# Optimization experiments

Hardware: AMD Instinct MI355X
Metric: run time of the kernel (lower is better)

## Reference

```python
import jax, jax.numpy as jnp
import numpy as np

N = 50000
E = 800000
IN_DIM = 128
HID_DIM = 128
OUT_DIM = 128
EPS = 1e-5


def setup_inputs() -> dict:
    key = jax.random.key(0)
    ks = jax.random.split(key, 6)
    x = jax.random.normal(ks[0], (N, IN_DIM), dtype=jnp.float32)
    src = jax.random.randint(ks[1], (E,), 0, N, dtype=jnp.int32)
    dst = jax.random.randint(ks[2], (E,), 0, N, dtype=jnp.int32)
    W1 = jax.random.normal(ks[3], (IN_DIM, HID_DIM), dtype=jnp.float32) / np.sqrt(IN_DIM)
    W2 = jax.random.normal(ks[4], (HID_DIM, OUT_DIM), dtype=jnp.float32) / np.sqrt(HID_DIM)
    return {
        "x": x, "src": src, "dst": dst,
        "W1": W1, "b1": jnp.zeros((HID_DIM,), jnp.float32),
        "gamma1": jnp.ones((HID_DIM,), jnp.float32), "beta1": jnp.zeros((HID_DIM,), jnp.float32),
        "W2": W2, "b2": jnp.zeros((OUT_DIM,), jnp.float32),
        "gamma2": jnp.ones((OUT_DIM,), jnp.float32), "beta2": jnp.zeros((OUT_DIM,), jnp.float32),
    }


def _degrees(src, dst, n):
    ones = jnp.ones(src.shape[0], jnp.float32)
    out_deg = jax.ops.segment_sum(ones, src, num_segments=n)
    in_deg = jax.ops.segment_sum(ones, dst, num_segments=n)
    # DGL norm='both' clamps degree to min 1 before pow(-0.5)
    return jnp.clip(out_deg, 1.0) ** -0.5, jnp.clip(in_deg, 1.0) ** -0.5


def _gconv(h, src, dst, d_out, d_in, W, b):
    h = h * d_out[:, None]                                   # [N, d] src-side norm
    m = jax.ops.segment_sum(h[src], dst, num_segments=h.shape[0])  # SpMM aggregate
    m = m * d_in[:, None]                                    # dst-side norm
    return m @ W + b


def _bn(h, gamma, beta):
    mu = jnp.mean(h, axis=0)
    var = jnp.var(h, axis=0)  # biased, matches torch BN training forward
    return gamma * (h - mu) * jax.lax.rsqrt(var + EPS) + beta


def reference(x, src, dst, W1, b1, gamma1, beta1, W2, b2, gamma2, beta2):
    d_out, d_in = _degrees(src, dst, x.shape[0])
    h1 = jax.nn.relu(_bn(_gconv(x, src, dst, d_out, d_in, W1, b1), gamma1, beta1))
    # dropout is identity in eval mode
    h2 = _bn(_gconv(h1, src, dst, d_out, d_in, W2, b2), gamma2, beta2)
    return jax.nn.relu(h2 + h1)
```

## Files before the change

### kernel.cpp

```cpp
#include <hip/hip_runtime.h>
#include <hip/hip_fp16.h>

#define NODES 50000
#define EDGES 800000
#define DIM 128
#define EPS_BN 1e-5f
#define SCAN_B 1024
#define SCAN_NB ((NODES + SCAN_B - 1) / SCAN_B)
#define GEMM_NB ((NODES + 63) / 64)
#define NCH 64
#define CHE (EDGES / NCH)
#define NR 4
#define RNG (NODES / NR)

typedef _Float16 half8 __attribute__((ext_vector_type(8)));
typedef float floatx4 __attribute__((ext_vector_type(4)));

__global__ __launch_bounds__(256) void hist_part_kernel(const int* __restrict__ src,
                                                        const int* __restrict__ dst,
                                                        unsigned short* __restrict__ Psrc,
                                                        unsigned short* __restrict__ Pdst) {
    __shared__ int h[RNG];
    int chunk = blockIdx.x & (NCH - 1);
    int range = blockIdx.x >> 6;
    const int* arr = blockIdx.y ? dst : src;
    unsigned short* P = blockIdx.y ? Pdst : Psrc;
    int base = range * RNG;
    for (int i = threadIdx.x; i < RNG; i += 256) h[i] = 0;
    __syncthreads();
    int e0 = chunk * CHE;
    for (int e = e0 + threadIdx.x; e < e0 + CHE; e += 256) {
        unsigned r = (unsigned)(arr[e] - base);
        if (r < (unsigned)RNG) atomicAdd(&h[r], 1);
    }
    __syncthreads();
    for (int i = threadIdx.x; i < RNG; i += 256)
        P[(size_t)chunk * NODES + base + i] = (unsigned short)h[i];
}

__global__ __launch_bounds__(256) void combine_kernel(const unsigned short* __restrict__ Psrc,
                                                      unsigned short* __restrict__ Pdst,
                                                      int* __restrict__ cnt_in,
                                                      float* __restrict__ dn_out,
                                                      float* __restrict__ dn_in) {
    int v = blockIdx.x * 256 + threadIdx.x;
    if (v >= NODES) return;
    int s = 0;
    #pragma unroll 8
    for (int j = 0; j < NCH; ++j) s += Psrc[(size_t)j * NODES + v];
    dn_out[v] = rsqrtf((float)max(s, 1));
    int run = 0;
    for (int j = 0; j < NCH; ++j) {
        int t = Pdst[(size_t)j * NODES + v];
        Pdst[(size_t)j * NODES + v] = (unsigned short)run;
        run += t;
    }
    cnt_in[v] = run;
    dn_in[v] = rsqrtf((float)max(run, 1));
}

__global__ __launch_bounds__(SCAN_B) void scan_p1_kernel(const int* __restrict__ cnt,
                                                         int* __restrict__ row_ptr,
                                                         int* __restrict__ blk_sums) {
    __shared__ int sm[SCAN_B];
    int t = threadIdx.x;
    int idx = blockIdx.x * SCAN_B + t;
    int v = (idx < NODES) ? cnt[idx] : 0;
    sm[t] = v;
    __syncthreads();
    #pragma unroll
    for (int off = 1; off < SCAN_B; off <<= 1) {
        int u = (t >= off) ? sm[t - off] : 0;
        __syncthreads();
        sm[t] += u;
        __syncthreads();
    }
    if (idx < NODES) row_ptr[idx] = sm[t] - v;
    if (t == SCAN_B - 1) blk_sums[blockIdx.x] = sm[t];
}

__global__ __launch_bounds__(64) void scan_p2_kernel(const int* __restrict__ blk_sums,
                                                     int* __restrict__ blk_off) {
    int t = threadIdx.x;
    int orig = (t < SCAN_NB) ? blk_sums[t] : 0;
    int v = orig;
    #pragma unroll
    for (int off = 1; off < 64; off <<= 1) {
        int u = __shfl_up(v, off);
        if (t >= off) v += u;
    }
    if (t < SCAN_NB) blk_off[t] = v - orig;
}

__global__ __launch_bounds__(SCAN_B) void scan_p3_kernel(int* __restrict__ row_ptr,
                                                         const int* __restrict__ blk_off) {
    int t = threadIdx.x;
    int idx = blockIdx.x * SCAN_B + t;
    if (idx < NODES) row_ptr[idx] += blk_off[blockIdx.x];
    if (idx == 0) row_ptr[NODES] = EDGES;
}

__global__ __launch_bounds__(256) void fill_kernel(const int* __restrict__ src,
                                                   const int* __restrict__ dst,
                                                   const int* __restrict__ row_ptr,
                                                   const unsigned short* __restrict__ Pdst,
                                                   int* __restrict__ csr_src) {
    __shared__ int h[RNG];
    int chunk = blockIdx.x & (NCH - 1);
    int range = blockIdx.x >> 6;
    int base = range * RNG;
    for (int i = threadIdx.x; i < RNG; i += 256) h[i] = 0;
    __syncthreads();
    int e0 = chunk * CHE;
    const unsigned short* Pj = Pdst + (size_t)chunk * NODES;
    for (int e = e0 + threadIdx.x; e < e0 + CHE; e += 256) {
        int d = dst[e];
        unsigned r = (unsigned)(d - base);
        if (r < (unsigned)RNG) {
            int local = atomicAdd(&h[r], 1);
            csr_src[row_ptr[d] + (int)Pj[d] + local] = src[e];
        }
    }
}

__global__ __launch_bounds__(256) void w2h_kernel(const float* __restrict__ W,
                                                  __half* __restrict__ WhT) {
    int idx = blockIdx.x * 256 + threadIdx.x;
    int n = idx >> 7;
    int k = idx & 127;
    WhT[idx] = __float2half(W[k * DIM + n]);
}

__global__ __launch_bounds__(256) void prescale_kernel(const float* __restrict__ x,
                                                       const float* __restrict__ dn_out,
                                                       __half* __restrict__ hs) {
    size_t idx = (size_t)blockIdx.x * 256 + threadIdx.x;
    if (idx >= (size_t)NODES * 32) return;
    int row = (int)(idx >> 5);
    float sc = dn_out[row];
    float4 v = *(const float4*)(x + idx * 4);
    __half2 a = __floats2half2_rn(v.x * sc, v.y * sc);
    __half2 b = __floats2half2_rn(v.z * sc, v.w * sc);
    float2 o;
    *(__half2*)&o.x = a;
    *(__half2*)&o.y = b;
    *(float2*)((char*)hs + idx * 8) = o;
}

__device__ __forceinline__ void acc_h4(float2 raw, float& ax, float& ay, float& az, float& aw) {
    __half2 p0 = *(__half2*)&raw.x;
    __half2 p1 = *(__half2*)&raw.y;
    float2 f0 = __half22float2(p0);
    float2 f1 = __half22float2(p1);
    ax += f0.x; ay += f0.y; az += f1.x; aw += f1.y;
}

__global__ __launch_bounds__(256) void pull_kernel(const __half* __restrict__ hs,
                                                   const int* __restrict__ row_ptr,
                                                   const int* __restrict__ csr_src,
                                                   const float* __restrict__ dn_in,
                                                   __half* __restrict__ agg) {
    int wid = threadIdx.x >> 6;
    int node = blockIdx.x * 4 + wid;
    if (node >= NODES) return;
    int lane = threadIdx.x & 63;
    int half = lane >> 5;
    int f4 = (lane & 31) * 4;
    const char* base = (const char*)hs;
    int beg = row_ptr[node];
    int end = row_ptr[node + 1];
    float ax = 0.f, ay = 0.f, az = 0.f, aw = 0.f;
    int e = beg + half;
    for (; e + 6 < end; e += 8) {
        int s0 = csr_src[e];
        int s1 = csr_src[e + 2];
        int s2 = csr_src[e + 4];
        int s3 = csr_src[e + 6];
        float2 r0 = *(const float2*)(base + ((size_t)s0 * DIM + f4) * 2);
        float2 r1 = *(const float2*)(base + ((size_t)s1 * DIM + f4) * 2);
        float2 r2 = *(const float2*)(base + ((size_t)s2 * DIM + f4) * 2);
        float2 r3 = *(const float2*)(base + ((size_t)s3 * DIM + f4) * 2);
        acc_h4(r0, ax, ay, az, aw);
        acc_h4(r1, ax, ay, az, aw);
        acc_h4(r2, ax, ay, az, aw);
        acc_h4(r3, ax, ay, az, aw);
    }
    for (; e < end; e += 2) {
        int s0 = csr_src[e];
        float2 r0 = *(const float2*)(base + ((size_t)s0 * DIM + f4) * 2);
        acc_h4(r0, ax, ay, az, aw);
    }
    ax += __shfl_xor(ax, 32);
    ay += __shfl_xor(ay, 32);
    az += __shfl_xor(az, 32);
    aw += __shfl_xor(aw, 32);
    if (half == 0) {
        float sc = dn_in[node];
        __half2 a = __floats2half2_rn(ax * sc, ay * sc);
        __half2 b = __floats2half2_rn(az * sc, aw * sc);
        float2 o;
        *(__half2*)&o.x = a;
        *(__half2*)&o.y = b;
        *(float2*)((char*)agg + ((size_t)node * DIM + f4) * 2) = o;
    }
}

__global__ __launch_bounds__(256) void gemm_mfma_kernel(const __half* __restrict__ A,
                                                        const __half* __restrict__ WhT,
                                                        const float* __restrict__ bias,
                                                        float* __restrict__ out,
                                                        float* __restrict__ partial) {
    __shared__ float smem[8704];
    __half* wl = (__half*)smem;

    int t = threadIdx.x;

    #pragma unroll
    for (int i = 0; i < 8; ++i) {
        int c = t + 256 * i;
        int n = c >> 4;
        int ch = c & 15;
        *(float4*)((char*)wl + n * 272 + ch * 16) =
            *(const float4*)((const char*)WhT + n * 256 + ch * 16);
    }

    int w = t >> 6;
    int lane = t & 63;
    int m = lane & 15;
    int quad = lane >> 4;
    int r0 = blockIdx.x * 64 + w * 16;
    int arow = r0 + m;

    half8 afrag[4];
    if (arow < NODES) {
        const char* ap = (const char*)(A + (size_t)arow * DIM);
        #pragma unroll
        for (int kt = 0; kt < 4; ++kt)
            afrag[kt] = *(const half8*)(ap + kt * 64 + quad * 16);
    } else {
        #pragma unroll
        for (int kt = 0; kt < 4; ++kt)
            #pragma unroll
            for (int j = 0; j < 8; ++j)
                afrag[kt][j] = (_Float16)0.0f;
    }

    floatx4 acc[8];
    floatx4 zf = {0.f, 0.f, 0.f, 0.f};
    #pragma unroll
    for (int ct = 0; ct < 8; ++ct) acc[ct] = zf;

    __syncthreads();

    #pragma unroll
    for (int kt = 0; kt < 4; ++kt) {
        #pragma unroll
        for (int ct = 0; ct < 8; ++ct) {
            half8 b = *(const half8*)((const char*)wl + (ct * 16 + m) * 272 + kt * 64 + quad * 16);
            acc[ct] = __builtin_amdgcn_mfma_f32_16x16x32_f16(afrag[kt], b, acc[ct], 0, 0, 0);
        }
    }

    __syncthreads();

    float* ps = smem;
    int g = w * 4 + quad;
    #pragma unroll
    for (int ct = 0; ct < 8; ++ct) {
        int col = ct * 16 + m;
        float bb = bias[col];
        float cs = 0.f, cq = 0.f;
        #pragma unroll
        for (int reg = 0; reg < 4; ++reg) {
            int row = r0 + quad * 4 + reg;
            if (row < NODES) {
                float o = acc[ct][reg] + bb;
                out[(size_t)row * DIM + col] = o;
                cs += o;
                cq += o * o;
            }
        }
        ps[g * 128 + col] = cs;
        ps[2048 + g * 128 + col] = cq;
    }
    __syncthreads();

    if (t < 128) {
        float s = 0.f;
        #pragma unroll
        for (int gg = 0; gg < 16; ++gg) s += ps[gg * 128 + t];
        partial[(size_t)blockIdx.x * 256 + t] = s;
    } else {
        int c = t - 128;
        float s = 0.f;
        #pragma unroll
        for (int gg = 0; gg < 16; ++gg) s += ps[2048 + gg * 128 + c];
        partial[(size_t)blockIdx.x * 256 + 128 + c] = s;
    }
}

__global__ __launch_bounds__(256) void stats_s1_kernel(const float* __restrict__ partial,
                                                       float* __restrict__ p2) {
    int t = threadIdx.x;
    float s = 0.f;
    for (int b = blockIdx.x; b < GEMM_NB; b += 32) s += partial[(size_t)b * 256 + t];
    p2[blockIdx.x * 256 + t] = s;
}

__global__ __launch_bounds__(256) void stats_s2_kernel(const float* __restrict__ p2,
                                                       float* __restrict__ stats) {
    int t = threadIdx.x;
    float s = 0.f;
    #pragma unroll
    for (int b = 0; b < 32; ++b) s += p2[b * 256 + t];
    stats[t] = s;
}

__global__ __launch_bounds__(256) void bn_relu_scale_kernel(float* __restrict__ h,
                                                            __half* __restrict__ hs,
                                                            const float* __restrict__ stats,
                                                            const float* __restrict__ g,
                                                            const float* __restrict__ be,
                                                            const float* __restrict__ dn_out) {
    size_t idx = (size_t)blockIdx.x * 256 + threadIdx.x;
    if (idx >= (size_t)NODES * 32) return;
    int c = (int)(idx & 31) * 4;
    int row = (int)(idx >> 5);
    const float invN = 1.0f / NODES;
    float4 v = *(float4*)(h + idx * 4);
    float vv[4] = {v.x, v.y, v.z, v.w};
    float o[4];
    #pragma unroll
    for (int j = 0; j < 4; ++j) {
        float mu = stats[c + j] * invN;
        float var = stats[DIM + c + j] * invN - mu * mu;
        float w = g[c + j] * rsqrtf(var + EPS_BN);
        o[j] = fmaxf(w * (vv[j] - mu) + be[c + j], 0.f);
    }
    float4 r = {o[0], o[1], o[2], o[3]};
    *(float4*)(h + idx * 4) = r;
    float sc = dn_out[row];
    __half2 a = __floats2half2_rn(o[0] * sc, o[1] * sc);
    __half2 b = __floats2half2_rn(o[2] * sc, o[3] * sc);
    float2 rs;
    *(__half2*)&rs.x = a;
    *(__half2*)&rs.y = b;
    *(float2*)((char*)hs + idx * 8) = rs;
}

__global__ __launch_bounds__(256) void bn_res_relu_kernel(float* __restrict__ out,
                                                          const float* __restrict__ h1,
                                                          const float* __restrict__ stats,
                                                          const float* __restrict__ g,
                                                          const float* __restrict__ be) {
    size_t idx = (size_t)blockIdx.x * 256 + threadIdx.x;
    if (idx >= (size_t)NODES * 32) return;
    int c = (int)(idx & 31) * 4;
    const float invN = 1.0f / NODES;
    float4 v = *(float4*)(out + idx * 4);
    float4 r1 = *(const float4*)(h1 + idx * 4);
    float vv[4] = {v.x, v.y, v.z, v.w};
    float rr[4] = {r1.x, r1.y, r1.z, r1.w};
    float o[4];
    #pragma unroll
    for (int j = 0; j < 4; ++j) {
        float mu = stats[c + j] * invN;
        float var = stats[DIM + c + j] * invN - mu * mu;
        float w = g[c + j] * rsqrtf(var + EPS_BN);
        o[j] = fmaxf(w * (vv[j] - mu) + be[c + j] + rr[j], 0.f);
    }
    float4 r = {o[0], o[1], o[2], o[3]};
    *(float4*)(out + idx * 4) = r;
}

extern "C" void kernel_launch(void* const* d_in, const int* in_sizes, int n_in,
                              void* d_out, int out_size, void* d_ws, size_t ws_size,
                              hipStream_t stream) {
    const float* x      = (const float*)d_in[0];
    const int*   src    = (const int*)d_in[1];
    const int*   dst    = (const int*)d_in[2];
    const float* W1     = (const float*)d_in[3];
    const float* b1     = (const float*)d_in[4];
    const float* gamma1 = (const float*)d_in[5];
    const float* beta1  = (const float*)d_in[6];
    const float* W2     = (const float*)d_in[7];
    const float* b2     = (const float*)d_in[8];
    const float* gamma2 = (const float*)d_in[9];
    const float* beta2  = (const float*)d_in[10];
    float* out = (float*)d_out;
    __half* hs = (__half*)d_out;

    char* wsc = (char*)d_ws;
    int*   cnt_in   = (int*)wsc;                     wsc += NODES * 4;
    float* dn_out   = (float*)wsc;                   wsc += NODES * 4;
    float* dn_in    = (float*)wsc;                   wsc += NODES * 4;
    int*   row_ptr  = (int*)wsc;                     wsc += (NODES + 1) * 4;
    int*   csr_src  = (int*)wsc;                     wsc += EDGES * 4;
    float* stats    = (float*)wsc;                   wsc += 2 * DIM * 4;
    int*   blk_sums = (int*)wsc;                     wsc += 64 * 4;
    int*   blk_off  = (int*)wsc;                     wsc += 64 * 4;
    __half* WhT1    = (__half*)wsc;                  wsc += DIM * DIM * 2;
    __half* WhT2    = (__half*)wsc;                  wsc += DIM * DIM * 2;
    float* partial  = (float*)wsc;                   wsc += (size_t)GEMM_NB * 256 * 4;
    float* p2       = (float*)wsc;                   wsc += 32 * 256 * 4;
    unsigned short* Psrc = (unsigned short*)wsc;     wsc += (size_t)NCH * NODES * 2;
    unsigned short* Pdst = (unsigned short*)wsc;     wsc += (size_t)NCH * NODES * 2;
    __half* agg     = (__half*)wsc;                  wsc += (size_t)NODES * DIM * 2;
    float* h1       = (float*)wsc;

    const int T = 256;
    const int grid_pull = (NODES + 3) / 4;
    const int grid_elem = (NODES * 32 + T - 1) / T;

    hist_part_kernel<<<dim3(NR * NCH, 2), T, 0, stream>>>(src, dst, Psrc, Pdst);
    combine_kernel<<<(NODES + T - 1) / T, T, 0, stream>>>(Psrc, Pdst, cnt_in, dn_out, dn_in);
    scan_p1_kernel<<<SCAN_NB, SCAN_B, 0, stream>>>(cnt_in, row_ptr, blk_sums);
    scan_p2_kernel<<<1, 64, 0, stream>>>(blk_sums, blk_off);
    scan_p3_kernel<<<SCAN_NB, SCAN_B, 0, stream>>>(row_ptr, blk_off);
    fill_kernel<<<NR * NCH, T, 0, stream>>>(src, dst, row_ptr, Pdst, csr_src);

    w2h_kernel<<<64, T, 0, stream>>>(W1, WhT1);
    w2h_kernel<<<64, T, 0, stream>>>(W2, WhT2);

    prescale_kernel<<<grid_elem, T, 0, stream>>>(x, dn_out, hs);
    pull_kernel<<<grid_pull, T, 0, stream>>>(hs, row_ptr, csr_src, dn_in, agg);
    gemm_mfma_kernel<<<GEMM_NB, T, 0, stream>>>(agg, WhT1, b1, h1, partial);
    stats_s1_kernel<<<32, T, 0, stream>>>(partial, p2);
    stats_s2_kernel<<<1, T, 0, stream>>>(p2, stats);
    bn_relu_scale_kernel<<<grid_elem, T, 0, stream>>>(h1, hs, stats, gamma1, beta1, dn_out);

    pull_kernel<<<grid_pull, T, 0, stream>>>(hs, row_ptr, csr_src, dn_in, agg);
    gemm_mfma_kernel<<<GEMM_NB, T, 0, stream>>>(agg, WhT2, b2, out, partial);
    stats_s1_kernel<<<32, T, 0, stream>>>(partial, p2);
    stats_s2_kernel<<<1, T, 0, stream>>>(p2, stats);
    bn_res_relu_kernel<<<grid_elem, T, 0, stream>>>(out, h1, stats, gamma2, beta2);
}
```

Before: 299.9 us.

## Store intermediates in fp16, widen gathers to 16 bytes, merge small kernels

The GEMM output and the layer-1 activation are now stored as fp16 instead of fp32, which halves the traffic of the elementwise BN kernels. The pull kernel gathers 16-byte half8 rows, with four edges processed in parallel per wavefront. The scan's second pass is folded into the third, and the two weight-conversion launches are merged into one. Storing pre-BN activations in fp16 adds rounding error in exchange for less memory traffic.

```diff
diff --git a/kernel.cpp b/kernel.cpp
--- a/kernel.cpp
+++ b/kernel.cpp
@@ -15,6 +15,8 @@
 
 typedef _Float16 half8 __attribute__((ext_vector_type(8)));
 typedef float floatx4 __attribute__((ext_vector_type(4)));
+
+union H8 { half8 v; __half2 h2[4]; };
 
 __global__ __launch_bounds__(256) void hist_part_kernel(const int* __restrict__ src,
                                                         const int* __restrict__ dst,
@@ -79,24 +81,19 @@
     if (t == SCAN_B - 1) blk_sums[blockIdx.x] = sm[t];
 }
 
-__global__ __launch_bounds__(64) void scan_p2_kernel(const int* __restrict__ blk_sums,
-                                                     int* __restrict__ blk_off) {
+__global__ __launch_bounds__(SCAN_B) void scan_p3_kernel(int* __restrict__ row_ptr,
+                                                         const int* __restrict__ blk_sums) {
+    __shared__ int soff;
     int t = threadIdx.x;
-    int orig = (t < SCAN_NB) ? blk_sums[t] : 0;
-    int v = orig;
-    #pragma unroll
-    for (int off = 1; off < 64; off <<= 1) {
-        int u = __shfl_up(v, off);
-        if (t >= off) v += u;
-    }
-    if (t < SCAN_NB) blk_off[t] = v - orig;
-}
-
-__global__ __launch_bounds__(SCAN_B) void scan_p3_kernel(int* __restrict__ row_ptr,
-                                                         const int* __restrict__ blk_off) {
-    int t = threadIdx.x;
+    if (t < 64) {
+        int v = (t < blockIdx.x) ? blk_sums[t] : 0;
+        #pragma unroll
+        for (int off = 32; off > 0; off >>= 1) v += __shfl_xor(v, off);
+        if (t == 0) soff = v;
+    }
+    __syncthreads();
     int idx = blockIdx.x * SCAN_B + t;
-    if (idx < NODES) row_ptr[idx] += blk_off[blockIdx.x];
+    if (idx < NODES) row_ptr[idx] += soff;
     if (idx == 0) row_ptr[NODES] = EDGES;
 }
 
@@ -123,36 +120,46 @@
     }
 }
 
-__global__ __launch_bounds__(256) void w2h_kernel(const float* __restrict__ W,
-                                                  __half* __restrict__ WhT) {
+__global__ __launch_bounds__(256) void w2h_kernel(const float* __restrict__ W1,
+                                                  const float* __restrict__ W2,
+                                                  __half* __restrict__ WhT1,
+                                                  __half* __restrict__ WhT2) {
     int idx = blockIdx.x * 256 + threadIdx.x;
-    int n = idx >> 7;
-    int k = idx & 127;
-    WhT[idx] = __float2half(W[k * DIM + n]);
+    const float* W = (idx < 16384) ? W1 : W2;
+    __half* D = (idx < 16384) ? WhT1 : WhT2;
+    int i = idx & 16383;
+    int n = i >> 7;
+    int k = i & 127;
+    D[i] = __float2half(W[k * DIM + n]);
 }
 
 __global__ __launch_bounds__(256) void prescale_kernel(const float* __restrict__ x,
                                                        const float* __restrict__ dn_out,
                                                        __half* __restrict__ hs) {
-    size_t idx = (size_t)blockIdx.x * 256 + threadIdx.x;
-    if (idx >= (size_t)NODES * 32) return;
-    int row = (int)(idx >> 5);
+    int idx = blockIdx.x * 256 + threadIdx.x;
+    if (idx >= NODES * 16) return;
+    int row = idx >> 4;
+    int c8 = (idx & 15) * 8;
     float sc = dn_out[row];
-    float4 v = *(const float4*)(x + idx * 4);
-    __half2 a = __floats2half2_rn(v.x * sc, v.y * sc);
-    __half2 b = __floats2half2_rn(v.z * sc, v.w * sc);
-    float2 o;
-    *(__half2*)&o.x = a;
-    *(__half2*)&o.y = b;
-    *(float2*)((char*)hs + idx * 8) = o;
-}
-
-__device__ __forceinline__ void acc_h4(float2 raw, float& ax, float& ay, float& az, float& aw) {
-    __half2 p0 = *(__half2*)&raw.x;
-    __half2 p1 = *(__half2*)&raw.y;
-    float2 f0 = __half22float2(p0);
-    float2 f1 = __half22float2(p1);
-    ax += f0.x; ay += f0.y; az += f1.x; aw += f1.y;
+    const float* xp = x + (size_t)row * DIM + c8;
+    float4 v0 = *(const float4*)xp;
+    float4 v1 = *(const float4*)(xp + 4);
+    H8 u;
+    u.h2[0] = __floats2half2_rn(v0.x * sc, v0.y * sc);
+    u.h2[1] = __floats2half2_rn(v0.z * sc, v0.w * sc);
+    u.h2[2] = __floats2half2_rn(v1.x * sc, v1.y * sc);
+    u.h2[3] = __floats2half2_rn(v1.z * sc, v1.w * sc);
+    *(half8*)((char*)hs + ((size_t)row * DIM + c8) * 2) = u.v;
+}
+
+__device__ __forceinline__ void acc_h8(half8 raw, float* a) {
+    H8 u; u.v = raw;
+    #pragma unroll
+    for (int k = 0; k < 4; ++k) {
+        float2 f = __half22float2(u.h2[k]);
+        a[2 * k] += f.x;
+        a[2 * k + 1] += f.y;
+    }
 }
 
 __global__ __launch_bounds__(256) void pull_kernel(const __half* __restrict__ hs,
@@ -164,51 +171,51 @@
     int node = blockIdx.x * 4 + wid;
     if (node >= NODES) return;
     int lane = threadIdx.x & 63;
-    int half = lane >> 5;
-    int f4 = (lane & 31) * 4;
+    int q = lane >> 4;
+    int c = lane & 15;
     const char* base = (const char*)hs;
     int beg = row_ptr[node];
     int end = row_ptr[node + 1];
-    float ax = 0.f, ay = 0.f, az = 0.f, aw = 0.f;
-    int e = beg + half;
-    for (; e + 6 < end; e += 8) {
-        int s0 = csr_src[e];
-        int s1 = csr_src[e + 2];
-        int s2 = csr_src[e + 4];
-        int s3 = csr_src[e + 6];
-        float2 r0 = *(const float2*)(base + ((size_t)s0 * DIM + f4) * 2);
-        float2 r1 = *(const float2*)(base + ((size_t)s1 * DIM + f4) * 2);
-        float2 r2 = *(const float2*)(base + ((size_t)s2 * DIM + f4) * 2);
-        float2 r3 = *(const float2*)(base + ((size_t)s3 * DIM + f4) * 2);
-        acc_h4(r0, ax, ay, az, aw);
-        acc_h4(r1, ax, ay, az, aw);
-        acc_h4(r2, ax, ay, az, aw);
-        acc_h4(r3, ax, ay, az, aw);
-    }
-    for (; e < end; e += 2) {
-        int s0 = csr_src[e];
-        float2 r0 = *(const float2*)(base + ((size_t)s0 * DIM + f4) * 2);
-        acc_h4(r0, ax, ay, az, aw);
-    }
-    ax += __shfl_xor(ax, 32);
-    ay += __shfl_xor(ay, 32);
-    az += __shfl_xor(az, 32);
-    aw += __shfl_xor(aw, 32);
-    if (half == 0) {
+    float a[8];
+    #pragma unroll
+    for (int i = 0; i < 8; ++i) a[i] = 0.f;
+    int eb = beg;
+    for (; eb + 8 <= end; eb += 8) {
+        int s0 = csr_src[eb + q];
+        int s1 = csr_src[eb + 4 + q];
+        half8 v0 = *(const half8*)(base + (size_t)s0 * 256 + c * 16);
+        half8 v1 = *(const half8*)(base + (size_t)s1 * 256 + c * 16);
+        acc_h8(v0, a);
+        acc_h8(v1, a);
+    }
+    for (; eb + 4 <= end; eb += 4) {
+        int s0 = csr_src[eb + q];
+        half8 v0 = *(const half8*)(base + (size_t)s0 * 256 + c * 16);
+        acc_h8(v0, a);
+    }
+    if (eb + q < end) {
+        int s0 = csr_src[eb + q];
+        half8 v0 = *(const half8*)(base + (size_t)s0 * 256 + c * 16);
+        acc_h8(v0, a);
+    }
+    #pragma unroll
+    for (int i = 0; i < 8; ++i) a[i] += __shfl_xor(a[i], 32);
+    #pragma unroll
+    for (int i = 0; i < 8; ++i) a[i] += __shfl_xor(a[i], 16);
+    if (lane < 16) {
         float sc = dn_in[node];
-        __half2 a = __floats2half2_rn(ax * sc, ay * sc);
-        __half2 b = __floats2half2_rn(az * sc, aw * sc);
-        float2 o;
-        *(__half2*)&o.x = a;
-        *(__half2*)&o.y = b;
-        *(float2*)((char*)agg + ((size_t)node * DIM + f4) * 2) = o;
+        H8 u;
+        #pragma unroll
+        for (int k = 0; k < 4; ++k)
+            u.h2[k] = __floats2half2_rn(a[2 * k] * sc, a[2 * k + 1] * sc);
+        *(half8*)((char*)agg + (size_t)node * 256 + c * 16) = u.v;
     }
 }
 
 __global__ __launch_bounds__(256) void gemm_mfma_kernel(const __half* __restrict__ A,
                                                         const __half* __restrict__ WhT,
                                                         const float* __restrict__ bias,
-                                                        float* __restrict__ out,
+                                                        __half* __restrict__ hraw,
                                                         float* __restrict__ partial) {
     __shared__ float smem[8704];
     __half* wl = (__half*)smem;
@@ -217,9 +224,9 @@
 
     #pragma unroll
     for (int i = 0; i < 8; ++i) {
-        int c = t + 256 * i;
-        int n = c >> 4;
-        int ch = c & 15;
+        int cch = t + 256 * i;
+        int n = cch >> 4;
+        int ch = cch & 15;
         *(float4*)((char*)wl + n * 272 + ch * 16) =
             *(const float4*)((const char*)WhT + n * 256 + ch * 16);
     }
@@ -275,7 +282,7 @@
             int row = r0 + quad * 4 + reg;
             if (row < NODES) {
                 float o = acc[ct][reg] + bb;
-                out[(size_t)row * DIM + col] = o;
+                hraw[(size_t)row * DIM + col] = __float2half(o);
                 cs += o;
                 cq += o * o;
             }
@@ -291,11 +298,11 @@
         for (int gg = 0; gg < 16; ++gg) s += ps[gg * 128 + t];
         partial[(size_t)blockIdx.x * 256 + t] = s;
     } else {
-        int c = t - 128;
+        int cc = t - 128;
         float s = 0.f;
         #pragma unroll
-        for (int gg = 0; gg < 16; ++gg) s += ps[2048 + gg * 128 + c];
-        partial[(size_t)blockIdx.x * 256 + 128 + c] = s;
+        for (int gg = 0; gg < 16; ++gg) s += ps[2048 + gg * 128 + cc];
+        partial[(size_t)blockIdx.x * 256 + 128 + cc] = s;
     }
 }
 
@@ -316,61 +323,81 @@
     stats[t] = s;
 }
 
-__global__ __launch_bounds__(256) void bn_relu_scale_kernel(float* __restrict__ h,
+__global__ __launch_bounds__(256) void bn_relu_scale_kernel(const __half* __restrict__ hraw,
+                                                            __half* __restrict__ h1r,
                                                             __half* __restrict__ hs,
                                                             const float* __restrict__ stats,
                                                             const float* __restrict__ g,
                                                             const float* __restrict__ be,
                                                             const float* __restrict__ dn_out) {
-    size_t idx = (size_t)blockIdx.x * 256 + threadIdx.x;
-    if (idx >= (size_t)NODES * 32) return;
-    int c = (int)(idx & 31) * 4;
-    int row = (int)(idx >> 5);
+    int idx = blockIdx.x * 256 + threadIdx.x;
+    if (idx >= NODES * 16) return;
+    int row = idx >> 4;
+    int c8 = (idx & 15) * 8;
     const float invN = 1.0f / NODES;
-    float4 v = *(float4*)(h + idx * 4);
-    float vv[4] = {v.x, v.y, v.z, v.w};
-    float o[4];
-    #pragma unroll
-    for (int j = 0; j < 4; ++j) {
-        float mu = stats[c + j] * invN;
-        float var = stats[DIM + c + j] * invN - mu * mu;
-        float w = g[c + j] * rsqrtf(var + EPS_BN);
-        o[j] = fmaxf(w * (vv[j] - mu) + be[c + j], 0.f);
-    }
-    float4 r = {o[0], o[1], o[2], o[3]};
-    *(float4*)(h + idx * 4) = r;
+    H8 u;
+    u.v = *(const half8*)((const char*)hraw + ((size_t)row * DIM + c8) * 2);
+    float o[8];
+    #pragma unroll
+    for (int k = 0; k < 4; ++k) {
+        float2 f = __half22float2(u.h2[k]);
+        o[2 * k] = f.x;
+        o[2 * k + 1] = f.y;
+    }
+    #pragma unroll
+    for (int j = 0; j < 8; ++j) {
+        int cj = c8 + j;
+        float mu = stats[cj] * invN;
+        float var = stats[DIM + cj] * invN - mu * mu;
+        float w = g[cj] * rsqrtf(var + EPS_BN);
+        o[j] = fmaxf(w * (o[j] - mu) + be[cj], 0.f);
+    }
+    H8 ur, us;
     float sc = dn_out[row];
-    __half2 a = __floats2half2_rn(o[0] * sc, o[1] * sc);
-    __half2 b = __floats2half2_rn(o[2] * sc, o[3] * sc);
-    float2 rs;
-    *(__half2*)&rs.x = a;
-    *(__half2*)&rs.y = b;
-    *(float2*)((char*)hs + idx * 8) = rs;
-}
-
-__global__ __launch_bounds__(256) void bn_res_relu_kernel(float* __restrict__ out,
-                                                          const float* __restrict__ h1,
+    #pragma unroll
+    for (int k = 0; k < 4; ++k) {
+        ur.h2[k] = __floats2half2_rn(o[2 * k], o[2 * k + 1]);
+        us.h2[k] = __floats2half2_rn(o[2 * k] * sc, o[2 * k + 1] * sc);
+    }
+    *(half8*)((char*)h1r + ((size_t)row * DIM + c8) * 2) = ur.v;
+    *(half8*)((char*)hs + ((size_t)row * DIM + c8) * 2) = us.v;
+}
+
+__global__ __launch_bounds__(256) void bn_res_relu_kernel(const __half* __restrict__ hraw,
+                                                          const __half* __restrict__ h1r,
+                                                          float* __restrict__ out,
                                                           const float* __restrict__ stats,
                                                           const float* __restrict__ g,
                                                           const float* __restrict__ be) {
-    size_t idx = (size_t)blockIdx.x * 256 + threadIdx.x;
-    if (idx >= (size_t)NODES * 32) return;
-    int c = (int)(idx & 31) * 4;
+    int idx = blockIdx.x * 256 + threadIdx.x;
+    if (idx >= NODES * 16) return;
+    int row = idx >> 4;
+    int c8 = (idx & 15) * 8;
     const float invN = 1.0f / NODES;
-    float4 v = *(float4*)(out + idx * 4);
-    float4 r1 = *(const float4*)(h1 + idx * 4);
-    float vv[4] = {v.x, v.y, v.z, v.w};
-    float rr[4] = {r1.x, r1.y, r1.z, r1.w};
-    float o[4];
-    #pragma unroll
-    for (int j = 0; j < 4; ++j) {
-        float mu = stats[c + j] * invN;
-        float var = stats[DIM + c + j] * invN - mu * mu;
-        float w = g[c + j] * rsqrtf(var + EPS_BN);
-        o[j] = fmaxf(w * (vv[j] - mu) + be[c + j] + rr[j], 0.f);
-    }
-    float4 r = {o[0], o[1], o[2], o[3]};
-    *(float4*)(out + idx * 4) = r;
+    H8 u, ur;
+    u.v = *(const half8*)((const char*)hraw + ((size_t)row * DIM + c8) * 2);
+    ur.v = *(const half8*)((const char*)h1r + ((size_t)row * DIM + c8) * 2);
+    float o[8], r[8];
+    #pragma unroll
+    for (int k = 0; k < 4; ++k) {
+        float2 f = __half22float2(u.h2[k]);
+        float2 fr = __half22float2(ur.h2[k]);
+        o[2 * k] = f.x; o[2 * k + 1] = f.y;
+        r[2 * k] = fr.x; r[2 * k + 1] = fr.y;
+    }
+    #pragma unroll
+    for (int j = 0; j < 8; ++j) {
+        int cj = c8 + j;
+        float mu = stats[cj] * invN;
+        float var = stats[DIM + cj] * invN - mu * mu;
+        float w = g[cj] * rsqrtf(var + EPS_BN);
+        o[j] = fmaxf(w * (o[j] - mu) + be[cj] + r[j], 0.f);
+    }
+    float* op = out + (size_t)row * DIM + c8;
+    float4 o0 = {o[0], o[1], o[2], o[3]};
+    float4 o1 = {o[4], o[5], o[6], o[7]};
+    *(float4*)op = o0;
+    *(float4*)(op + 4) = o1;
 }
 
 extern "C" void kernel_launch(void* const* d_in, const int* in_sizes, int n_in,
@@ -398,7 +425,6 @@
     int*   csr_src  = (int*)wsc;                     wsc += EDGES * 4;
     float* stats    = (float*)wsc;                   wsc += 2 * DIM * 4;
     int*   blk_sums = (int*)wsc;                     wsc += 64 * 4;
-    int*   blk_off  = (int*)wsc;                     wsc += 64 * 4;
     __half* WhT1    = (__half*)wsc;                  wsc += DIM * DIM * 2;
     __half* WhT2    = (__half*)wsc;                  wsc += DIM * DIM * 2;
     float* partial  = (float*)wsc;                   wsc += (size_t)GEMM_NB * 256 * 4;
@@ -406,32 +432,31 @@
     unsigned short* Psrc = (unsigned short*)wsc;     wsc += (size_t)NCH * NODES * 2;
     unsigned short* Pdst = (unsigned short*)wsc;     wsc += (size_t)NCH * NODES * 2;
     __half* agg     = (__half*)wsc;                  wsc += (size_t)NODES * DIM * 2;
-    float* h1       = (float*)wsc;
+    __half* hraw    = (__half*)wsc;                  wsc += (size_t)NODES * DIM * 2;
+    __half* h1r     = (__half*)wsc;                  wsc += (size_t)NODES * DIM * 2;
 
     const int T = 256;
     const int grid_pull = (NODES + 3) / 4;
-    const int grid_elem = (NODES * 32 + T - 1) / T;
+    const int grid_e16  = (NODES * 16 + T - 1) / T;
 
     hist_part_kernel<<<dim3(NR * NCH, 2), T, 0, stream>>>(src, dst, Psrc, Pdst);
     combine_kernel<<<(NODES + T - 1) / T, T, 0, stream>>>(Psrc, Pdst, cnt_in, dn_out, dn_in);
     scan_p1_kernel<<<SCAN_NB, SCAN_B, 0, stream>>>(cnt_in, row_ptr, blk_sums);
-    scan_p2_kernel<<<1, 64, 0, stream>>>(blk_sums, blk_off);
-    scan_p3_kernel<<<SCAN_NB, SCAN_B, 0, stream>>>(row_ptr, blk_off);
+    scan_p3_kernel<<<SCAN_NB, SCAN_B, 0, stream>>>(row_ptr, blk_sums);
     fill_kernel<<<NR * NCH, T, 0, stream>>>(src, dst, row_ptr, Pdst, csr_src);
 
-    w2h_kernel<<<64, T, 0, stream>>>(W1, WhT1);
-    w2h_kernel<<<64, T, 0, stream>>>(W2, WhT2);
-
-    prescale_kernel<<<grid_elem, T, 0, stream>>>(x, dn_out, hs);
+    w2h_kernel<<<128, T, 0, stream>>>(W1, W2, WhT1, WhT2);
+
+    prescale_kernel<<<grid_e16, T, 0, stream>>>(x, dn_out, hs);
     pull_kernel<<<grid_pull, T, 0, stream>>>(hs, row_ptr, csr_src, dn_in, agg);
-    gemm_mfma_kernel<<<GEMM_NB, T, 0, stream>>>(agg, WhT1, b1, h1, partial);
+    gemm_mfma_kernel<<<GEMM_NB, T, 0, stream>>>(agg, WhT1, b1, hraw, partial);
     stats_s1_kernel<<<32, T, 0, stream>>>(partial, p2);
     stats_s2_kernel<<<1, T, 0, stream>>>(p2, stats);
-    bn_relu_scale_kernel<<<grid_elem, T, 0, stream>>>(h1, hs, stats, gamma1, beta1, dn_out);
+    bn_relu_scale_kernel<<<grid_e16, T, 0, stream>>>(hraw, h1r, hs, stats, gamma1, beta1, dn_out);
 
     pull_kernel<<<grid_pull, T, 0, stream>>>(hs, row_ptr, csr_src, dn_in, agg);
-    gemm_mfma_kernel<<<GEMM_NB, T, 0, stream>>>(agg, WhT2, b2, out, partial);
+    gemm_mfma_kernel<<<GEMM_NB, T, 0, stream>>>(agg, WhT2, b2, hraw, partial);
     stats_s1_kernel<<<32, T, 0, stream>>>(partial, p2);
     stats_s2_kernel<<<1, T, 0, stream>>>(p2, stats);
-    bn_res_relu_kernel<<<grid_elem, T, 0, stream>>>(out, h1, stats, gamma2, beta2);
-}
+    bn_res_relu_kernel<<<grid_e16, T, 0, stream>>>(hraw, h1r, out, stats, gamma2, beta2);
+}
```

Result: faster. 283.7 us (-5.4%).
